# Kernel optimization log

Measured on AMD Instinct MI355X. Metric: run time of the kernel, lower is better.

The kernel has to match this reference:

```python
import jax, jax.numpy as jnp
import numpy as np

C = 64
SIZE = 448
PATCH = 14
P2 = PATCH * PATCH                 # 196, per-chunk token count
SPLIT = (SIZE * SIZE) // P2        # 1024 chunks
TG = PATCH * 4                     # 56, pooled global resolution
POOL = SIZE // TG                  # 8, exact avg-pool factor
EPS = 1e-5


def setup_inputs() -> dict:
    key = jax.random.key(0)
    ks = jax.random.split(key, 10)
    b = 2
    x = jax.random.normal(ks[0], (b, C, SIZE, SIZE), dtype=jnp.float32)
    s = 1.0 / np.sqrt(C)
    return {
        "x": x,
        "gn_w": jnp.ones((C,), jnp.float32),
        "gn_b": jnp.zeros((C,), jnp.float32),
        "q_w": jax.random.normal(ks[1], (C, C), jnp.float32) * s,
        "q_b": jnp.zeros((C,), jnp.float32),
        "k_w": jax.random.normal(ks[2], (C, C), jnp.float32) * s,
        "k_b": jnp.zeros((C,), jnp.float32),
        "v_w": jax.random.normal(ks[3], (C, C), jnp.float32) * s,
        "v_b": jnp.zeros((C,), jnp.float32),
        "proj_w": jax.random.normal(ks[4], (C, C), jnp.float32) * s,
    }


def _conv1x1(t, W, bias=None):
    out = jnp.einsum('oc,bchw->bohw', W, t)
    if bias is not None:
        out = out + bias[None, :, None, None]
    return out


def _group_norm(x, w, b):
    # GroupNorm(num_groups=1): normalize over (C,H,W) per sample
    mean = x.mean(axis=(1, 2, 3), keepdims=True)
    var = x.var(axis=(1, 2, 3), keepdims=True)
    xn = (x - mean) * jax.lax.rsqrt(var + EPS)
    return xn * w[None, :, None, None] + b[None, :, None, None]


def reference(x, gn_w, gn_b, q_w, q_b, k_w, k_b, v_w, v_b, proj_w):
    b, c, h, w = x.shape
    xn = _group_norm(x, gn_w, gn_b)
    q = _conv1x1(xn, q_w, q_b)
    k = _conv1x1(xn, k_w, k_b)
    v = _conv1x1(xn, v_w, v_b)

    # ---- patch-local attention (channels*chunks as feature dim S) ----
    S = c * SPLIT  # 65536
    qf = q.reshape(b, S, P2)
    kf = k.reshape(b, S, P2)
    vf = v.reshape(b, S, P2)
    wm = jnp.einsum('bsp,bsq->bpq', qf, kf) * (S ** -0.5)  # [b,196,196]
    wm = jax.nn.softmax(wm, axis=2)
    # h[b,s,q'] = sum_k v[b,s,k] * wm[b,q',k]
    hp = jnp.einsum('bsk,bqk->bsq', vf, wm).reshape(b, c, h, w)

    # ---- global pooled attention ----
    pool = lambda t: t.reshape(b, c, TG, POOL, TG, POOL).mean(axis=(3, 5))
    qg = pool(q).reshape(b, c, TG * TG)
    kg = pool(k).reshape(b, c, TG * TG)
    vg = pool(v).reshape(b, c, TG * TG)
    wg = jnp.einsum('bcp,bcq->bpq', qg, kg) * (c ** -0.5)  # [b,3136,3136]
    wg = jax.nn.softmax(wg, axis=2)
    hg = jnp.einsum('bck,bqk->bcq', vg, wg).reshape(b, c, TG, TG)
    hg = jnp.repeat(jnp.repeat(hg, POOL, axis=2), POOL, axis=3)

    h_in = 0.75 * hp + 0.25 * hg
    out = _conv1x1(h_in, proj_w)  # proj_out, no bias
    return x + out
```

## Files before the change

### kernel.cpp

```cpp
#include <hip/hip_runtime.h>

#define NB 2
#define NC 64
#define HW 200704
#define CHW 12845056
#define P2 196
#define NCHUNK 1024
#define NCELL 3136
#define WMN 38416

typedef __attribute__((ext_vector_type(8))) short bfrag;
typedef __attribute__((ext_vector_type(4))) float ffrag;
typedef __attribute__((ext_vector_type(4))) short short4v;
typedef __attribute__((ext_vector_type(4))) float float4v;

#define MFMA16(A,B,C) __builtin_amdgcn_mfma_f32_16x16x32_bf16(A,B,C,0,0,0)

__device__ __forceinline__ short f2bf(float f) {
  unsigned u = __builtin_bit_cast(unsigned, f);
  u = u + 0x7FFFu + ((u >> 16) & 1u);
  return (short)(u >> 16);
}

__global__ __launch_bounds__(64) void k1_stats_pool(
    const float* __restrict__ x, float* __restrict__ xpool, float* __restrict__ partials) {
  int bx = blockIdx.x;
  int batch = bx / (64*56);
  int c = (bx / 56) % 64;
  int pr = bx % 56;
  int l = threadIdx.x;
  const float* xp = x + (size_t)batch*CHW + (size_t)c*HW + pr*8*448;
  float cell = 0.f, s2 = 0.f;
  if (l < 56) {
    #pragma unroll
    for (int r = 0; r < 8; ++r) {
      float4v a = *(const float4v*)(xp + r*448 + l*8);
      float4v b = *(const float4v*)(xp + r*448 + l*8 + 4);
      #pragma unroll
      for (int j = 0; j < 4; ++j) { cell += a[j] + b[j]; s2 += a[j]*a[j] + b[j]*b[j]; }
    }
    xpool[((size_t)batch*64 + c)*NCELL + pr*56 + l] = cell * (1.f/64.f);
  }
  float s1 = (l < 56) ? cell : 0.f;
  #pragma unroll
  for (int m = 1; m < 64; m <<= 1) { s1 += __shfl_xor(s1, m, 64); s2 += __shfl_xor(s2, m, 64); }
  if (l == 0) { partials[bx*2] = s1; partials[bx*2 + 1] = s2; }
}

__global__ __launch_bounds__(256) void k1b_reduce(
    const float* __restrict__ partials, float* __restrict__ stats) {
  __shared__ float red[2][256];
  int t = threadIdx.x;
  for (int b = 0; b < NB; ++b) {
    float s1 = 0.f, s2 = 0.f;
    for (int i = t; i < 3584; i += 256) {
      s1 += partials[(b*3584 + i)*2];
      s2 += partials[(b*3584 + i)*2 + 1];
    }
    red[0][t] = s1; red[1][t] = s2;
    __syncthreads();
    for (int m = 128; m > 0; m >>= 1) {
      if (t < m) { red[0][t] += red[0][t+m]; red[1][t] += red[1][t+m]; }
      __syncthreads();
    }
    if (t == 0) { stats[b*2] = red[0][0]; stats[b*2+1] = red[1][0]; }
    __syncthreads();
  }
}

__global__ __launch_bounds__(256) void k2_qkv(
    const float* __restrict__ x, const float* __restrict__ gnw, const float* __restrict__ gnb,
    const float* __restrict__ qw, const float* __restrict__ qb,
    const float* __restrict__ kw, const float* __restrict__ kb,
    const float* __restrict__ vw, const float* __restrict__ vb,
    const float* __restrict__ stats,
    short* __restrict__ qx, short* __restrict__ kx, short* __restrict__ vnat) {
  __shared__ __attribute__((aligned(16))) short xnt[256*72];
  int bx = blockIdx.x;
  int batch = bx / 784;
  int px0 = (bx % 784) * 256;
  int t = threadIdx.x;
  float s1 = stats[batch*2], s2 = stats[batch*2+1];
  float mean = s1 * (1.f/CHW);
  float rstd = rsqrtf(s2*(1.f/CHW) - mean*mean + 1e-5f);
  for (int it = 0; it < 64; it += 4) {
    float vv[4];
    #pragma unroll
    for (int r = 0; r < 4; ++r) {
      float v = x[(size_t)batch*CHW + (size_t)(it+r)*HW + px0 + t];
      vv[r] = (v - mean) * rstd * gnw[it+r] + gnb[it+r];
    }
    short4v s;
    #pragma unroll
    for (int r = 0; r < 4; ++r) s[r] = f2bf(vv[r]);
    *(short4v*)(xnt + t*72 + it) = s;
  }
  __syncthreads();
  int l = t & 63, w = t >> 6, li = l & 15, q_ = l >> 4;
  bfrag bfr[4][2];
  #pragma unroll
  for (int nn = 0; nn < 4; ++nn) {
    int row = (w*4 + nn)*16 + li;
    bfr[nn][0] = *(const bfrag*)(xnt + row*72 + q_*8);
    bfr[nn][1] = *(const bfrag*)(xnt + row*72 + 32 + q_*8);
  }
  const float* Ws[3] = {qw, kw, vw};
  const float* Bs[3] = {qb, kb, vb};
  for (int T = 0; T < 3; ++T) {
    ffrag acc[4][4];
    #pragma unroll
    for (int mt = 0; mt < 4; ++mt) {
      bfrag a0, a1;
      const float* wp = Ws[T] + (mt*16 + li)*64;
      #pragma unroll
      for (int j = 0; j < 8; ++j) { a0[j] = f2bf(wp[q_*8 + j]); a1[j] = f2bf(wp[32 + q_*8 + j]); }
      #pragma unroll
      for (int nn = 0; nn < 4; ++nn) {
        ffrag z = {0.f,0.f,0.f,0.f};
        z = MFMA16(a0, bfr[nn][0], z);
        z = MFMA16(a1, bfr[nn][1], z);
        acc[mt][nn] = z;
      }
    }
    if (T < 2) {
      short* dstb = (T == 0 ? qx : kx) + (size_t)batch*HW*64;
      #pragma unroll
      for (int nn = 0; nn < 4; ++nn) {
        int px = px0 + (w*4 + nn)*16 + li;
        #pragma unroll
        for (int mt = 0; mt < 4; ++mt) {
          float4v bias = *(const float4v*)(Bs[T] + mt*16 + q_*4);
          short4v s;
          #pragma unroll
          for (int r = 0; r < 4; ++r) s[r] = f2bf(acc[mt][nn][r] + bias[r]);
          *(short4v*)(dstb + (size_t)px*64 + mt*16 + q_*4) = s;
        }
      }
    } else {
      #pragma unroll
      for (int nn = 0; nn < 4; ++nn) {
        int px = px0 + (w*4 + nn)*16 + li;
        #pragma unroll
        for (int mt = 0; mt < 4; ++mt) {
          float4v bias = *(const float4v*)(Bs[T] + mt*16 + q_*4);
          #pragma unroll
          for (int r = 0; r < 4; ++r) {
            int c = mt*16 + q_*4 + r;
            vnat[((size_t)batch*64 + c)*HW + px] = f2bf(acc[mt][nn][r] + bias[r]);
          }
        }
      }
    }
  }
}

__global__ __launch_bounds__(256) void k2a_pool_qkv(
    const float* __restrict__ xpool, const float* __restrict__ stats,
    const float* __restrict__ gnw, const float* __restrict__ gnb,
    const float* __restrict__ qw, const float* __restrict__ qb,
    const float* __restrict__ kw, const float* __restrict__ kb,
    const float* __restrict__ vw, const float* __restrict__ vb,
    short* __restrict__ qgt, short* __restrict__ kgt, short* __restrict__ vgn) {
  __shared__ float xs[64][64];
  int bx = blockIdx.x;
  int batch = bx / 49;
  int j0 = (bx % 49) * 64;
  int t = threadIdx.x;
  float s1 = stats[batch*2], s2 = stats[batch*2+1];
  float mean = s1 * (1.f/CHW);
  float rstd = rsqrtf(s2*(1.f/CHW) - mean*mean + 1e-5f);
  #pragma unroll
  for (int it = 0; it < 16; ++it) {
    int idx = t + it*256;
    int c = idx >> 6, jl = idx & 63;
    float v = xpool[((size_t)batch*64 + c)*NCELL + j0 + jl];
    xs[c][jl] = (v - mean)*rstd*gnw[c] + gnb[c];
  }
  __syncthreads();
  int jl = t & 63;
  int og = (t >> 6) * 16;
  int j = j0 + jl;
  for (int T = 0; T < 3; ++T) {
    const float* W  = (T==0 ? qw : (T==1 ? kw : vw));
    const float* Bv = (T==0 ? qb : (T==1 ? kb : vb));
    float o16[16];
    #pragma unroll
    for (int oo = 0; oo < 16; ++oo) o16[oo] = Bv[og+oo];
    for (int c = 0; c < 64; ++c) {
      float xv = xs[c][jl];
      #pragma unroll
      for (int oo = 0; oo < 16; ++oo) o16[oo] += W[(og+oo)*64 + c] * xv;
    }
    if (T < 2) {
      short* dst = (T==0 ? qgt : kgt) + ((size_t)batch*NCELL + j)*64 + og;
      #pragma unroll
      for (int oo = 0; oo < 16; oo += 4) {
        short4v s;
        #pragma unroll
        for (int r = 0; r < 4; ++r) s[r] = f2bf(o16[oo+r]);
        *(short4v*)(dst + oo) = s;
      }
    } else {
      #pragma unroll
      for (int oo = 0; oo < 16; ++oo)
        vgn[((size_t)batch*64 + og + oo)*NCELL + j] = f2bf(o16[oo]);
    }
  }
}

__global__ __launch_bounds__(512) void k3_wm(
    const short* __restrict__ qx, const short* __restrict__ kx, float* __restrict__ wmacc) {
  int bx = blockIdx.x;
  int batch = bx >> 6;
  int slab = bx & 63;
  int t = threadIdx.x;
  int l = t & 63, w = t >> 6, li = l & 15, q_ = l >> 4;
  int wm_ = w >> 2, wn = w & 3;
  int m0 = wm_ * 7, mcnt = wm_ ? 6 : 7;
  int nt0 = wn ? 4 + (wn-1)*3 : 0, ncnt = wn ? 3 : 4;
  ffrag acc[7][4];
  #pragma unroll
  for (int i = 0; i < 7; ++i)
    #pragma unroll
    for (int j = 0; j < 4; ++j) acc[i][j] = (ffrag){0.f,0.f,0.f,0.f};
  const short* qbase = qx + (size_t)batch*HW*64;
  const short* kbase = kx + (size_t)batch*HW*64;
  for (int c8 = 0; c8 < 16; ++c8) {
    int chunk = slab*16 + c8;
    const short* qc = qbase + (size_t)chunk*P2*64;
    const short* kc = kbase + (size_t)chunk*P2*64;
    #pragma unroll
    for (int ks = 0; ks < 2; ++ks) {
      int koff = ks*32 + q_*8;
      bfrag af[7], bf[4];
      #pragma unroll
      for (int mi = 0; mi < 7; ++mi) if (mi < mcnt)
        af[mi] = *(const bfrag*)(qc + (size_t)((m0+mi)*16 + li)*64 + koff);
      #pragma unroll
      for (int ni = 0; ni < 4; ++ni) if (ni < ncnt)
        bf[ni] = *(const bfrag*)(kc + (size_t)((nt0+ni)*16 + li)*64 + koff);
      #pragma unroll
      for (int mi = 0; mi < 7; ++mi) if (mi < mcnt)
        #pragma unroll
        for (int ni = 0; ni < 4; ++ni) if (ni < ncnt)
          acc[mi][ni] = MFMA16(af[mi], bf[ni], acc[mi][ni]);
    }
  }
  float* wdst = wmacc + (size_t)batch*WMN;
  #pragma unroll
  for (int mi = 0; mi < 7; ++mi) if (mi < mcnt)
    #pragma unroll
    for (int ni = 0; ni < 4; ++ni) if (ni < ncnt) {
      int qcol = (nt0+ni)*16 + li;
      if (qcol < 196)
        #pragma unroll
        for (int r = 0; r < 4; ++r) {
          int prow = (m0+mi)*16 + q_*4 + r;
          if (prow < 196) atomicAdd(wdst + prow*196 + qcol, acc[mi][ni][r]);
        }
    }
}

__global__ __launch_bounds__(64) void k4_softmax(
    const float* __restrict__ wmacc, short* __restrict__ P) {
  int bx = blockIdx.x;
  int batch = bx / 208;
  int p = bx % 208;
  int l = threadIdx.x;
  short* prow = P + ((size_t)batch*208 + p)*224;
  if (p >= 196) { for (int j = l; j < 224; j += 64) prow[j] = 0; return; }
  const float* src = wmacc + (size_t)batch*WMN + p*196;
  float v[4]; float mx = -1e30f;
  #pragma unroll
  for (int i = 0; i < 4; ++i) {
    int q = l + i*64;
    v[i] = (q < 196) ? src[q]*(1.f/256.f) : -1e30f;
    mx = fmaxf(mx, v[i]);
  }
  #pragma unroll
  for (int m = 1; m < 64; m <<= 1) mx = fmaxf(mx, __shfl_xor(mx, m, 64));
  float s = 0.f;
  #pragma unroll
  for (int i = 0; i < 4; ++i) { v[i] = __expf(v[i] - mx); s += v[i]; }
  #pragma unroll
  for (int m = 1; m < 64; m <<= 1) s += __shfl_xor(s, m, 64);
  float inv = 1.f / s;
  #pragma unroll
  for (int i = 0; i < 4; ++i) {
    int q = l + i*64;
    if (q < 224) prow[q] = (q < 196) ? f2bf(v[i]*inv) : (short)0;
  }
}

__global__ __launch_bounds__(256) void k5_gattn(
    const short* __restrict__ qgt, const short* __restrict__ kgt,
    const short* __restrict__ vgn, float* __restrict__ hgt) {
  __shared__ __attribute__((aligned(16))) short Pl[4][16][72];
  __shared__ __attribute__((aligned(16))) float alph[4][16];
  __shared__ __attribute__((aligned(16))) float Om[4][16][64];
  __shared__ __attribute__((aligned(16))) float ml[4][2][16];
  int bx = blockIdx.x;
  int batch = bx / 196;
  int i0 = (bx % 196) * 16;
  int t = threadIdx.x;
  int w = t >> 6, l = t & 63, li = l & 15, q_ = l >> 4;
  const short* qg = qgt + (size_t)batch*NCELL*64;
  const short* kg = kgt + (size_t)batch*NCELL*64;
  const short* vg = vgn + (size_t)batch*64*NCELL;
  bfrag bq0 = *(const bfrag*)(qg + (size_t)(i0+li)*64 + q_*8);
  bfrag bq1 = *(const bfrag*)(qg + (size_t)(i0+li)*64 + 32 + q_*8);
  float m_run = -1e30f, l_run = 0.f;
  ffrag oa[4];
  #pragma unroll
  for (int i = 0; i < 4; ++i) oa[i] = (ffrag){0.f,0.f,0.f,0.f};
  for (int jt = w; jt < 49; jt += 4) {
    int j0 = jt*64;
    ffrag st[4];
    #pragma unroll
    for (int mt = 0; mt < 4; ++mt) {
      bfrag a0 = *(const bfrag*)(kg + (size_t)(j0 + mt*16 + li)*64 + q_*8);
      bfrag a1 = *(const bfrag*)(kg + (size_t)(j0 + mt*16 + li)*64 + 32 + q_*8);
      ffrag z = {0.f,0.f,0.f,0.f};
      z = MFMA16(a0, bq0, z);
      z = MFMA16(a1, bq1, z);
      st[mt] = z;
    }
    float mx = -1e30f;
    #pragma unroll
    for (int mt = 0; mt < 4; ++mt)
      #pragma unroll
      for (int r = 0; r < 4; ++r) { st[mt][r] *= 0.125f; mx = fmaxf(mx, st[mt][r]); }
    mx = fmaxf(mx, __shfl_xor(mx, 16, 64));
    mx = fmaxf(mx, __shfl_xor(mx, 32, 64));
    float m_new = fmaxf(m_run, mx);
    float alpha = __expf(m_run - m_new);
    float ps = 0.f;
    short4v pk[4];
    #pragma unroll
    for (int mt = 0; mt < 4; ++mt)
      #pragma unroll
      for (int r = 0; r < 4; ++r) { float e = __expf(st[mt][r] - m_new); ps += e; pk[mt][r] = f2bf(e); }
    ps += __shfl_xor(ps, 16, 64);
    ps += __shfl_xor(ps, 32, 64);
    l_run = l_run*alpha + ps;
    m_run = m_new;
    #pragma unroll
    for (int mt = 0; mt < 4; ++mt) *(short4v*)(&Pl[w][li][mt*16 + q_*4]) = pk[mt];
    alph[w][li] = alpha;
    float4v al = *(const float4v*)(&alph[w][q_*4]);
    #pragma unroll
    for (int nt = 0; nt < 4; ++nt)
      #pragma unroll
      for (int r = 0; r < 4; ++r) oa[nt][r] *= al[r];
    #pragma unroll
    for (int ks = 0; ks < 2; ++ks) {
      bfrag a = *(const bfrag*)(&Pl[w][li][ks*32 + q_*8]);
      #pragma unroll
      for (int nt = 0; nt < 4; ++nt) {
        bfrag b = *(const bfrag*)(vg + (size_t)(nt*16 + li)*NCELL + j0 + ks*32 + q_*8);
        oa[nt] = MFMA16(a, b, oa[nt]);
      }
    }
  }
  ml[w][0][li] = m_run;
  ml[w][1][li] = l_run;
  #pragma unroll
  for (int nt = 0; nt < 4; ++nt)
    #pragma unroll
    for (int r = 0; r < 4; ++r)
      Om[w][q_*4 + r][nt*16 + li] = oa[nt][r];
  __syncthreads();
  int qq = t >> 4, c4 = (t & 15) * 4;
  float m0 = ml[0][0][qq], m1 = ml[1][0][qq], m2 = ml[2][0][qq], m3 = ml[3][0][qq];
  float ms = fmaxf(fmaxf(m0, m1), fmaxf(m2, m3));
  float s0 = __expf(m0 - ms), s1 = __expf(m1 - ms);
  float s2 = __expf(m2 - ms), s3 = __expf(m3 - ms);
  float lt = ml[0][1][qq]*s0 + ml[1][1][qq]*s1 + ml[2][1][qq]*s2 + ml[3][1][qq]*s3;
  float inv = 1.f / lt;
  float sw[4] = {s0, s1, s2, s3};
  float4v o = {0.f, 0.f, 0.f, 0.f};
  #pragma unroll
  for (int w2 = 0; w2 < 4; ++w2) {
    float4v ov = *(const float4v*)(&Om[w2][qq][c4]);
    #pragma unroll
    for (int r = 0; r < 4; ++r) o[r] += ov[r] * sw[w2];
  }
  float4v outv;
  #pragma unroll
  for (int r = 0; r < 4; ++r) outv[r] = o[r] * inv;
  *(float4v*)(hgt + (size_t)batch*NCELL*64 + (size_t)(i0 + qq)*64 + c4) = outv;
}

__global__ __launch_bounds__(256) void k6_hp_proj(
    const short* __restrict__ vnat, const short* __restrict__ P,
    const float* __restrict__ hgt, const float* __restrict__ projw,
    const float* __restrict__ x, float* __restrict__ out) {
  __shared__ __attribute__((aligned(16))) short smem[208*72];
  short* vch = smem;
  short* hl  = smem;
  float* fs  = (float*)smem;
  int bx = blockIdx.x;
  int batch = bx >> 10;
  int chunk = bx & 1023;
  int t = threadIdx.x;
  const short* vsrc = vnat + (size_t)batch*64*HW + chunk*P2;
  for (int idx = t; idx < 3136; idx += 256) {
    int c = idx / 49, po = idx % 49;
    *(short4v*)(vch + c*232 + po*4) = *(const short4v*)(vsrc + (size_t)c*HW + po*4);
  }
  for (int idx = t; idx < 448; idx += 256) {
    int c = idx / 7, po = idx % 7;
    *(short4v*)(vch + c*232 + 196 + po*4) = (short4v){0,0,0,0};
  }
  __syncthreads();
  int l = t & 63, w = t >> 6, li = l & 15, q_ = l >> 4;
  int nt0 = w ? 4 + (w-1)*3 : 0;
  int ncnt = w ? 3 : 4;
  const short* Pb = P + (size_t)batch*208*224;
  ffrag acc[4][4];
  #pragma unroll
  for (int i = 0; i < 4; ++i)
    #pragma unroll
    for (int j = 0; j < 4; ++j) acc[i][j] = (ffrag){0.f,0.f,0.f,0.f};
  #pragma unroll
  for (int ks = 0; ks < 7; ++ks) {
    int koff = ks*32 + q_*8;
    bfrag av[4];
    #pragma unroll
    for (int mt = 0; mt < 4; ++mt) av[mt] = *(const bfrag*)(vch + (mt*16 + li)*232 + koff);
    #pragma unroll
    for (int ni = 0; ni < 4; ++ni) if (ni < ncnt) {
      bfrag bp = *(const bfrag*)(Pb + (size_t)((nt0+ni)*16 + li)*224 + koff);
      #pragma unroll
      for (int mt = 0; mt < 4; ++mt) acc[mt][ni] = MFMA16(av[mt], bp, acc[mt][ni]);
    }
  }
  __syncthreads();
  const float* hgb = hgt + (size_t)batch*NCELL*64;
  #pragma unroll
  for (int ni = 0; ni < 4; ++ni) if (ni < ncnt) {
    int pp = (nt0+ni)*16 + li;
    if (pp < 196) {
      int g = chunk*P2 + pp;
      int hh = g / 448, ww_ = g % 448;
      int cell = (hh >> 3)*56 + (ww_ >> 3);
      #pragma unroll
      for (int mt = 0; mt < 4; ++mt) {
        float4v hgv = *(const float4v*)(hgb + (size_t)cell*64 + mt*16 + q_*4);
        short4v s;
        #pragma unroll
        for (int r = 0; r < 4; ++r) s[r] = f2bf(0.75f*acc[mt][ni][r] + 0.25f*hgv[r]);
        *(short4v*)(hl + pp*72 + mt*16 + q_*4) = s;
      }
    }
  }
  for (int idx = t; idx < 216; idx += 256) {
    int rr = 196 + idx/18, cc = (idx%18)*4;
    *(short4v*)(hl + rr*72 + cc) = (short4v){0,0,0,0};
  }
  __syncthreads();
  ffrag acc2[4][4];
  #pragma unroll
  for (int i = 0; i < 4; ++i)
    #pragma unroll
    for (int j = 0; j < 4; ++j) acc2[i][j] = (ffrag){0.f,0.f,0.f,0.f};
  #pragma unroll
  for (int ks = 0; ks < 2; ++ks) {
    bfrag aw[4];
    #pragma unroll
    for (int mt = 0; mt < 4; ++mt) {
      const float* wp = projw + (mt*16 + li)*64 + ks*32 + q_*8;
      #pragma unroll
      for (int j = 0; j < 8; ++j) aw[mt][j] = f2bf(wp[j]);
    }
    #pragma unroll
    for (int ni = 0; ni < 4; ++ni) if (ni < ncnt) {
      bfrag bh = *(const bfrag*)(hl + ((nt0+ni)*16 + li)*72 + ks*32 + q_*8);
      #pragma unroll
      for (int mt = 0; mt < 4; ++mt) acc2[mt][ni] = MFMA16(aw[mt], bh, acc2[mt][ni]);
    }
  }
  __syncthreads();
  const float* xb = x + (size_t)batch*CHW;
  float* ob = out + (size_t)batch*CHW;
  #pragma unroll
  for (int h = 0; h < 2; ++h) {
    #pragma unroll
    for (int ni = 0; ni < 4; ++ni) if (ni < ncnt) {
      int pp = (nt0+ni)*16 + li;
      if (pp < 196) {
        #pragma unroll
        for (int mt = 0; mt < 2; ++mt) {
          #pragma unroll
          for (int r = 0; r < 4; ++r)
            fs[(mt*16 + q_*4 + r)*204 + pp] = acc2[h*2 + mt][ni][r];
        }
      }
    }
    __syncthreads();
    for (int idx = t; idx < 32*49; idx += 256) {
      int c = idx / 49, po = idx % 49;
      size_t off = (size_t)(h*32 + c)*HW + (size_t)chunk*P2 + po*4;
      float4v xv = *(const float4v*)(xb + off);
      float4v fv = *(const float4v*)(fs + c*204 + po*4);
      float4v o;
      #pragma unroll
      for (int r = 0; r < 4; ++r) o[r] = xv[r] + fv[r];
      *(float4v*)(ob + off) = o;
    }
    __syncthreads();
  }
}

extern "C" void kernel_launch(void* const* d_in, const int* in_sizes, int n_in,
                              void* d_out, int out_size, void* d_ws, size_t ws_size,
                              hipStream_t stream) {
  (void)in_sizes; (void)n_in; (void)out_size; (void)ws_size;
  const float* x   = (const float*)d_in[0];
  const float* gnw = (const float*)d_in[1];
  const float* gnb = (const float*)d_in[2];
  const float* qw  = (const float*)d_in[3];
  const float* qb  = (const float*)d_in[4];
  const float* kw  = (const float*)d_in[5];
  const float* kb  = (const float*)d_in[6];
  const float* vw  = (const float*)d_in[7];
  const float* vb  = (const float*)d_in[8];
  const float* pw  = (const float*)d_in[9];
  float* out = (float*)d_out;
  char* ws = (char*)d_ws;

  short* qx    = (short*)(ws + 0);
  short* kx    = (short*)(ws + 51380224);
  short* vnat  = (short*)(ws + 102760448);
  float* xpool = (float*)(ws + 154140672);
  short* qgt   = (short*)(ws + 155746304);
  short* kgt   = (short*)(ws + 156549120);
  short* vgn   = (short*)(ws + 157351936);
  float* hgt   = (float*)(ws + 158154752);
  short* P     = (short*)(ws + 159760384);
  float* wmacc = (float*)(ws + 159946752);
  float* stats = (float*)(ws + 160254080);
  float* partials = (float*)(ws + 159760384);

  hipMemsetAsync(ws + 159946752, 0, 307328, stream);
  k1_stats_pool<<<dim3(NB*64*56), dim3(64),  0, stream>>>(x, xpool, partials);
  k1b_reduce   <<<dim3(1),        dim3(256), 0, stream>>>(partials, stats);
  k2_qkv       <<<dim3(NB*784),   dim3(256), 0, stream>>>(x, gnw, gnb, qw, qb, kw, kb, vw, vb, stats, qx, kx, vnat);
  k2a_pool_qkv <<<dim3(NB*49),    dim3(256), 0, stream>>>(xpool, stats, gnw, gnb, qw, qb, kw, kb, vw, vb, qgt, kgt, vgn);
  k3_wm        <<<dim3(NB*64),    dim3(512), 0, stream>>>(qx, kx, wmacc);
  k4_softmax   <<<dim3(NB*208),   dim3(64),  0, stream>>>(wmacc, P);
  k5_gattn     <<<dim3(NB*196),   dim3(256), 0, stream>>>(qgt, kgt, vgn, hgt);
  k6_hp_proj   <<<dim3(NB*1024),  dim3(256), 0, stream>>>(vnat, P, hgt, pw, x, out);
}
```

Measured before the change: 603.8 us.

## Fold proj_out weights into the V projection and drop the final GEMM

The output projection is linear and the attention weights are row-stochastic, so proj_w is pre-multiplied into v_w and v_b by a tiny new kernel. The V projections for both the patch and pooled paths then produce already-projected values. The last kernel therefore skips its second MFMA GEMM and its LDS staging, reading V fragments straight from global memory and blending with the global branch before the residual add. Separately, the k3 reduction grid is doubled so each block handles 8 chunks instead of 16, giving more parallelism at the cost of more atomic accumulation into the score buffer.

```diff
diff --git a/kernel.cpp b/kernel.cpp
--- a/kernel.cpp
+++ b/kernel.cpp
@@ -20,6 +20,28 @@
   unsigned u = __builtin_bit_cast(unsigned, f);
   u = u + 0x7FFFu + ((u >> 16) & 1u);
   return (short)(u >> 16);
+}
+
+__global__ __launch_bounds__(256) void k0_fold(
+    const float* __restrict__ pw, const float* __restrict__ vw,
+    const float* __restrict__ vb, float* __restrict__ wtld, float* __restrict__ btld) {
+  int t = threadIdx.x;
+  if (blockIdx.x == 0) {
+    #pragma unroll
+    for (int i = 0; i < 16; ++i) {
+      int idx = i*256 + t;
+      int o = idx >> 6, c = idx & 63;
+      float s = 0.f;
+      for (int m = 0; m < 64; ++m) s += pw[o*64 + m] * vw[m*64 + c];
+      wtld[o*64 + c] = s;
+    }
+  } else {
+    if (t < 64) {
+      float s = 0.f;
+      for (int m = 0; m < 64; ++m) s += pw[t*64 + m] * vb[m];
+      btld[t] = s;
+    }
+  }
 }
 
 __global__ __launch_bounds__(64) void k1_stats_pool(
@@ -211,8 +233,8 @@
 __global__ __launch_bounds__(512) void k3_wm(
     const short* __restrict__ qx, const short* __restrict__ kx, float* __restrict__ wmacc) {
   int bx = blockIdx.x;
-  int batch = bx >> 6;
-  int slab = bx & 63;
+  int batch = bx >> 7;
+  int slab = bx & 127;
   int t = threadIdx.x;
   int l = t & 63, w = t >> 6, li = l & 15, q_ = l >> 4;
   int wm_ = w >> 2, wn = w & 3;
@@ -225,8 +247,8 @@
     for (int j = 0; j < 4; ++j) acc[i][j] = (ffrag){0.f,0.f,0.f,0.f};
   const short* qbase = qx + (size_t)batch*HW*64;
   const short* kbase = kx + (size_t)batch*HW*64;
-  for (int c8 = 0; c8 < 16; ++c8) {
-    int chunk = slab*16 + c8;
+  for (int c8 = 0; c8 < 8; ++c8) {
+    int chunk = slab*8 + c8;
     const short* qc = qbase + (size_t)chunk*P2*64;
     const short* kc = kbase + (size_t)chunk*P2*64;
     #pragma unroll
@@ -391,32 +413,20 @@
   *(float4v*)(hgt + (size_t)batch*NCELL*64 + (size_t)(i0 + qq)*64 + c4) = outv;
 }
 
-__global__ __launch_bounds__(256) void k6_hp_proj(
-    const short* __restrict__ vnat, const short* __restrict__ P,
-    const float* __restrict__ hgt, const float* __restrict__ projw,
+__global__ __launch_bounds__(256) void k6_hp_out(
+    const short* __restrict__ vtld, const short* __restrict__ P,
+    const float* __restrict__ hgt,
     const float* __restrict__ x, float* __restrict__ out) {
-  __shared__ __attribute__((aligned(16))) short smem[208*72];
-  short* vch = smem;
-  short* hl  = smem;
-  float* fs  = (float*)smem;
+  __shared__ __attribute__((aligned(16))) float fs[16][204];
   int bx = blockIdx.x;
   int batch = bx >> 10;
   int chunk = bx & 1023;
   int t = threadIdx.x;
-  const short* vsrc = vnat + (size_t)batch*64*HW + chunk*P2;
-  for (int idx = t; idx < 3136; idx += 256) {
-    int c = idx / 49, po = idx % 49;
-    *(short4v*)(vch + c*232 + po*4) = *(const short4v*)(vsrc + (size_t)c*HW + po*4);
-  }
-  for (int idx = t; idx < 448; idx += 256) {
-    int c = idx / 7, po = idx % 7;
-    *(short4v*)(vch + c*232 + 196 + po*4) = (short4v){0,0,0,0};
-  }
-  __syncthreads();
   int l = t & 63, w = t >> 6, li = l & 15, q_ = l >> 4;
   int nt0 = w ? 4 + (w-1)*3 : 0;
   int ncnt = w ? 3 : 4;
   const short* Pb = P + (size_t)batch*208*224;
+  const short* vbase = vtld + (size_t)batch*64*HW + chunk*P2;
   ffrag acc[4][4];
   #pragma unroll
   for (int i = 0; i < 4; ++i)
@@ -427,7 +437,8 @@
     int koff = ks*32 + q_*8;
     bfrag av[4];
     #pragma unroll
-    for (int mt = 0; mt < 4; ++mt) av[mt] = *(const bfrag*)(vch + (mt*16 + li)*232 + koff);
+    for (int mt = 0; mt < 4; ++mt)
+      av[mt] = *(const bfrag*)(vbase + (size_t)(mt*16 + li)*HW + koff);
     #pragma unroll
     for (int ni = 0; ni < 4; ++ni) if (ni < ncnt) {
       bfrag bp = *(const bfrag*)(Pb + (size_t)((nt0+ni)*16 + li)*224 + koff);
@@ -435,74 +446,33 @@
       for (int mt = 0; mt < 4; ++mt) acc[mt][ni] = MFMA16(av[mt], bp, acc[mt][ni]);
     }
   }
-  __syncthreads();
+  int pp[4], cell[4];
+  #pragma unroll
+  for (int ni = 0; ni < 4; ++ni) {
+    pp[ni] = (nt0+ni)*16 + li;
+    int g = chunk*P2 + pp[ni];
+    cell[ni] = ((g / 448) >> 3)*56 + ((g % 448) >> 3);
+  }
   const float* hgb = hgt + (size_t)batch*NCELL*64;
-  #pragma unroll
-  for (int ni = 0; ni < 4; ++ni) if (ni < ncnt) {
-    int pp = (nt0+ni)*16 + li;
-    if (pp < 196) {
-      int g = chunk*P2 + pp;
-      int hh = g / 448, ww_ = g % 448;
-      int cell = (hh >> 3)*56 + (ww_ >> 3);
-      #pragma unroll
-      for (int mt = 0; mt < 4; ++mt) {
-        float4v hgv = *(const float4v*)(hgb + (size_t)cell*64 + mt*16 + q_*4);
-        short4v s;
-        #pragma unroll
-        for (int r = 0; r < 4; ++r) s[r] = f2bf(0.75f*acc[mt][ni][r] + 0.25f*hgv[r]);
-        *(short4v*)(hl + pp*72 + mt*16 + q_*4) = s;
-      }
-    }
-  }
-  for (int idx = t; idx < 216; idx += 256) {
-    int rr = 196 + idx/18, cc = (idx%18)*4;
-    *(short4v*)(hl + rr*72 + cc) = (short4v){0,0,0,0};
-  }
-  __syncthreads();
-  ffrag acc2[4][4];
-  #pragma unroll
-  for (int i = 0; i < 4; ++i)
-    #pragma unroll
-    for (int j = 0; j < 4; ++j) acc2[i][j] = (ffrag){0.f,0.f,0.f,0.f};
-  #pragma unroll
-  for (int ks = 0; ks < 2; ++ks) {
-    bfrag aw[4];
-    #pragma unroll
-    for (int mt = 0; mt < 4; ++mt) {
-      const float* wp = projw + (mt*16 + li)*64 + ks*32 + q_*8;
-      #pragma unroll
-      for (int j = 0; j < 8; ++j) aw[mt][j] = f2bf(wp[j]);
-    }
-    #pragma unroll
-    for (int ni = 0; ni < 4; ++ni) if (ni < ncnt) {
-      bfrag bh = *(const bfrag*)(hl + ((nt0+ni)*16 + li)*72 + ks*32 + q_*8);
-      #pragma unroll
-      for (int mt = 0; mt < 4; ++mt) acc2[mt][ni] = MFMA16(aw[mt], bh, acc2[mt][ni]);
-    }
-  }
-  __syncthreads();
   const float* xb = x + (size_t)batch*CHW;
   float* ob = out + (size_t)batch*CHW;
   #pragma unroll
-  for (int h = 0; h < 2; ++h) {
+  for (int mt = 0; mt < 4; ++mt) {
     #pragma unroll
     for (int ni = 0; ni < 4; ++ni) if (ni < ncnt) {
-      int pp = (nt0+ni)*16 + li;
-      if (pp < 196) {
+      if (pp[ni] < 196) {
+        float4v hgv = *(const float4v*)(hgb + (size_t)cell[ni]*64 + mt*16 + q_*4);
         #pragma unroll
-        for (int mt = 0; mt < 2; ++mt) {
-          #pragma unroll
-          for (int r = 0; r < 4; ++r)
-            fs[(mt*16 + q_*4 + r)*204 + pp] = acc2[h*2 + mt][ni][r];
-        }
+        for (int r = 0; r < 4; ++r)
+          fs[q_*4 + r][pp[ni]] = 0.75f*acc[mt][ni][r] + 0.25f*hgv[r];
       }
     }
     __syncthreads();
-    for (int idx = t; idx < 32*49; idx += 256) {
-      int c = idx / 49, po = idx % 49;
-      size_t off = (size_t)(h*32 + c)*HW + (size_t)chunk*P2 + po*4;
+    for (int idx = t; idx < 784; idx += 256) {
+      int c16 = idx / 49, po = idx % 49;
+      size_t off = (size_t)(mt*16 + c16)*HW + (size_t)chunk*P2 + po*4;
       float4v xv = *(const float4v*)(xb + off);
-      float4v fv = *(const float4v*)(fs + c*204 + po*4);
+      float4v fv = *(const float4v*)(&fs[c16][po*4]);
       float4v o;
       #pragma unroll
       for (int r = 0; r < 4; ++r) o[r] = xv[r] + fv[r];
@@ -541,14 +511,17 @@
   float* wmacc = (float*)(ws + 159946752);
   float* stats = (float*)(ws + 160254080);
   float* partials = (float*)(ws + 159760384);
+  float* wtld = (float*)(ws + 158154752);
+  float* btld = (float*)(ws + 158154752 + 16384);
 
   hipMemsetAsync(ws + 159946752, 0, 307328, stream);
+  k0_fold      <<<dim3(2),        dim3(256), 0, stream>>>(pw, vw, vb, wtld, btld);
   k1_stats_pool<<<dim3(NB*64*56), dim3(64),  0, stream>>>(x, xpool, partials);
   k1b_reduce   <<<dim3(1),        dim3(256), 0, stream>>>(partials, stats);
-  k2_qkv       <<<dim3(NB*784),   dim3(256), 0, stream>>>(x, gnw, gnb, qw, qb, kw, kb, vw, vb, stats, qx, kx, vnat);
-  k2a_pool_qkv <<<dim3(NB*49),    dim3(256), 0, stream>>>(xpool, stats, gnw, gnb, qw, qb, kw, kb, vw, vb, qgt, kgt, vgn);
-  k3_wm        <<<dim3(NB*64),    dim3(512), 0, stream>>>(qx, kx, wmacc);
+  k2_qkv       <<<dim3(NB*784),   dim3(256), 0, stream>>>(x, gnw, gnb, qw, qb, kw, kb, wtld, btld, stats, qx, kx, vnat);
+  k2a_pool_qkv <<<dim3(NB*49),    dim3(256), 0, stream>>>(xpool, stats, gnw, gnb, qw, qb, kw, kb, wtld, btld, qgt, kgt, vgn);
+  k3_wm        <<<dim3(NB*128),   dim3(512), 0, stream>>>(qx, kx, wmacc);
   k4_softmax   <<<dim3(NB*208),   dim3(64),  0, stream>>>(wmacc, P);
   k5_gattn     <<<dim3(NB*196),   dim3(256), 0, stream>>>(qgt, kgt, vgn, hgt);
-  k6_hp_proj   <<<dim3(NB*1024),  dim3(256), 0, stream>>>(vnat, P, hgt, pw, x, out);
-}
+  k6_hp_out    <<<dim3(NB*1024),  dim3(256), 0, stream>>>(vnat, P, hgt, x, out);
+}
```

Measured after the change: 637.4 us. +5.6%, slower.
